# Optimization experiments

Measured on AMD Instinct MI355X. Metric: run time of the kernel, lower is better.

## Reference

```python
import jax, jax.numpy as jnp
import numpy as np

K_H, K_W = 3, 3
STRIDE, PAD = 1, 1
GN_GROUPS = 32
EPS = 1e-5


def setup_inputs() -> dict:
    key = jax.random.key(0)
    k1, k2, k3 = jax.random.split(key, 3)
    B, C, H, W = 4, 256, 64, 64
    Cout = 256
    x = jax.random.normal(k1, (B, C, H, W), jnp.float32)
    offset = jax.random.normal(k2, (B, 2 * K_H * K_W, H, W), jnp.float32)
    weight = jax.random.normal(k3, (Cout, C, K_H, K_W), jnp.float32) * 0.02
    gamma = jnp.ones((Cout,), jnp.float32)
    beta = jnp.zeros((Cout,), jnp.float32)
    return {"x": x, "offset": offset, "weight": weight, "gamma": gamma, "beta": beta}


def _deform_conv(x, offset, weight):
    B, C, H, W = x.shape
    Cout = weight.shape[0]
    K = K_H * K_W
    Ho = (H + 2 * PAD - K_H) // STRIDE + 1
    Wo = (W + 2 * PAD - K_W) // STRIDE + 1
    ky, kx = jnp.meshgrid(jnp.arange(K_H), jnp.arange(K_W), indexing='ij')
    ky = ky.reshape(K).astype(x.dtype)
    kx = kx.reshape(K).astype(x.dtype)
    # base sampling positions per kernel tap
    py_base = (jnp.arange(Ho) * STRIDE - PAD).astype(x.dtype)[None, :] + ky[:, None]  # [K,Ho]
    px_base = (jnp.arange(Wo) * STRIDE - PAD).astype(x.dtype)[None, :] + kx[:, None]  # [K,Wo]
    off = offset.reshape(B, K, 2, Ho, Wo)  # mmcv layout: (dy, dx) pairs per tap
    py = py_base[None, :, :, None] + off[:, :, 0]  # [B,K,Ho,Wo]
    px = px_base[None, :, None, :] + off[:, :, 1]  # [B,K,Ho,Wo]
    y0 = jnp.floor(py)
    x0 = jnp.floor(px)
    ly = py - y0
    lx = px - x0
    xf = x.reshape(B, C, H * W)

    def gather(yi, xi):
        valid = (yi >= 0) & (yi <= H - 1) & (xi >= 0) & (xi <= W - 1)
        yc = jnp.clip(yi, 0, H - 1).astype(jnp.int32)
        xc = jnp.clip(xi, 0, W - 1).astype(jnp.int32)
        idx = yc * W + xc  # [B,K,Ho,Wo]
        vals = jax.vmap(lambda xb, ib: xb[:, ib])(xf, idx)  # [B,C,K,Ho,Wo]
        return vals * valid[:, None].astype(x.dtype)

    g00 = gather(y0, x0)
    g01 = gather(y0, x0 + 1)
    g10 = gather(y0 + 1, x0)
    g11 = gather(y0 + 1, x0 + 1)
    wy = ly[:, None]  # [B,1,K,Ho,Wo]
    wx = lx[:, None]
    val = ((1 - wy) * (1 - wx) * g00 + (1 - wy) * wx * g01
           + wy * (1 - wx) * g10 + wy * wx * g11)  # [B,C,K,Ho,Wo]
    return jnp.einsum('bckhw,ock->bohw', val, weight.reshape(Cout, C, K))


def reference(x, offset, weight, gamma, beta):
    y = _deform_conv(x, offset, weight)  # [B,Cout,Ho,Wo]
    B, C, H, W = y.shape
    yg = y.reshape(B, GN_GROUPS, C // GN_GROUPS, H, W)
    mean = jnp.mean(yg, axis=(2, 3, 4), keepdims=True)
    var = jnp.var(yg, axis=(2, 3, 4), keepdims=True)
    yn = ((yg - mean) * jax.lax.rsqrt(var + EPS)).reshape(B, C, H, W)
    out = yn * gamma[None, :, None, None] + beta[None, :, None, None]
    return jax.nn.relu(out)
```

## Files before the change

kernel.cpp:

```cpp
#include <hip/hip_runtime.h>

typedef unsigned short ushort_t;
typedef __bf16 bf16x8 __attribute__((ext_vector_type(8)));
typedef float f32x4 __attribute__((ext_vector_type(4)));
typedef void __attribute__((address_space(1))) gvoid_t;
typedef void __attribute__((address_space(3))) lvoid_t;

__device__ __forceinline__ float bflo(unsigned u) { return __builtin_bit_cast(float, u << 16); }
__device__ __forceinline__ float bfhi(unsigned u) { return __builtin_bit_cast(float, u & 0xffff0000u); }
__device__ __forceinline__ unsigned f2bf_bits(float f) {
  unsigned u = __builtin_bit_cast(unsigned, f);
  return (u + 0x7fffu + ((u >> 16) & 1u)) >> 16;
}
__device__ __forceinline__ ushort_t f2bf(float f) { return (ushort_t)f2bf_bits(f); }

__global__ __launch_bounds__(256) void k_prep_w(const float* __restrict__ w,
                                                ushort_t* __restrict__ wb) {
  const int idx = blockIdx.x * 256 + threadIdx.x;
  const float* src = w + (size_t)idx * 9;
  #pragma unroll
  for (int k = 0; k < 9; ++k)
    wb[(k << 16) + idx] = f2bf(src[k]);
}

__global__ __launch_bounds__(256) void k_prep_x(const float* __restrict__ x,
                                                ushort_t* __restrict__ xt) {
  __shared__ ushort_t tile[64][68];
  const int bid = blockIdx.x;
  const int b = bid >> 8;
  const int ct = (bid >> 6) & 3;
  const int pt = bid & 63;
  const int t = threadIdx.x;
  const float* xb = x + ((size_t)(b * 256 + ct * 64)) * 4096 + pt * 64;
  #pragma unroll
  for (int i = 0; i < 16; ++i) {
    const int idx = t + 256 * i;
    const int c_l = idx >> 6, p_l = idx & 63;
    tile[c_l][p_l] = f2bf(xb[(size_t)c_l * 4096 + p_l]);
  }
  __syncthreads();
  ushort_t* xo = xt + ((size_t)(b * 4096 + pt * 64)) * 256 + ct * 64;
  #pragma unroll
  for (int i = 0; i < 16; ++i) {
    const int idx = t + 256 * i;
    const int p_l = idx >> 6, c_l = idx & 63;
    xo[(size_t)p_l * 256 + c_l] = tile[c_l][p_l];
  }
}

struct SMeta {
  float w00, w01, w10, w11;
  int i00, i01, i10, i11;
};
__device__ __forceinline__ SMeta meta_for(int h, int gw, int k, float oy, float ox) {
  SMeta m;
  const float py = (float)(h - 1 + k / 3) + oy;
  const float px = (float)(gw - 1 + k % 3) + ox;
  const float fy = floorf(py), fx = floorf(px);
  const float ly = py - fy, lx = px - fx;
  const int iy0 = (int)fy, ix0 = (int)fx;
  const float vy0 = (iy0 >= 0 && iy0 < 64) ? 1.f : 0.f;
  const float vy1 = (iy0 >= -1 && iy0 < 63) ? 1.f : 0.f;
  const float vx0 = (ix0 >= 0 && ix0 < 64) ? 1.f : 0.f;
  const float vx1 = (ix0 >= -1 && ix0 < 63) ? 1.f : 0.f;
  m.w00 = (1.f - ly) * (1.f - lx) * vy0 * vx0;
  m.w01 = (1.f - ly) * lx * vy0 * vx1;
  m.w10 = ly * (1.f - lx) * vy1 * vx0;
  m.w11 = ly * lx * vy1 * vx1;
  const int cy0 = min(max(iy0, 0), 63), cy1 = min(max(iy0 + 1, 0), 63);
  const int cx0 = min(max(ix0, 0), 63), cx1 = min(max(ix0 + 1, 0), 63);
  m.i00 = (cy0 * 64 + cx0) * 256;
  m.i01 = (cy0 * 64 + cx1) * 256;
  m.i10 = (cy1 * 64 + cx0) * 256;
  m.i11 = (cy1 * 64 + cx1) * 256;
  return m;
}

__device__ __forceinline__ unsigned lerp_pack(unsigned a, unsigned b, unsigned c, unsigned d,
                                              float w00, float w01, float w10, float w11) {
  float lo = w00 * bflo(a) + w01 * bflo(b) + w10 * bflo(c) + w11 * bflo(d);
  float hi = w00 * bfhi(a) + w01 * bfhi(b) + w10 * bfhi(c) + w11 * bfhi(d);
  return f2bf_bits(lo) | (f2bf_bits(hi) << 16);
}

__global__ __launch_bounds__(512) void k_gemm(const float* __restrict__ off,
                                              const ushort_t* __restrict__ xt,
                                              const ushort_t* __restrict__ wb,
                                              float* __restrict__ y,
                                              float* __restrict__ stats) {
  __shared__ __attribute__((aligned(16))) ushort_t Abuf[2][64 * 64];
  __shared__ __attribute__((aligned(16))) ushort_t Bbuf[2][256 * 64];

  const int bid = blockIdx.x;
  const int b = bid >> 6;
  const int h = bid & 63;
  const int t = threadIdx.x;
  const int wave = t >> 6;
  const int lane = t & 63;
  const int wq = lane >> 4;
  const int wr = lane & 15;
  const int wm = wave >> 2;
  const int wn = wave & 3;

  const int s_w = t >> 3;
  const int c8 = t & 7;

  const f32x4 zero = {0.f, 0.f, 0.f, 0.f};
  f32x4 acc[2][4];
  #pragma unroll
  for (int i = 0; i < 2; ++i)
    #pragma unroll
    for (int j = 0; j < 4; ++j) acc[i][j] = zero;

  const ushort_t* xtb = xt + (size_t)b * 4096 * 256;

  float offy[9], offx[9];
  {
    const float* offb = off + (size_t)b * 18 * 4096 + h * 64 + s_w;
    #pragma unroll
    for (int k = 0; k < 9; ++k) {
      offy[k] = offb[(2 * k) * 4096];
      offx[k] = offb[(2 * k + 1) * 4096];
    }
  }

  {
    const SMeta m = meta_for(h, s_w, 0, offy[0], offx[0]);
    const int cc = c8 * 8;
    const uint4 q00 = *(const uint4*)(xtb + m.i00 + cc);
    const uint4 q01 = *(const uint4*)(xtb + m.i01 + cc);
    const uint4 q10 = *(const uint4*)(xtb + m.i10 + cc);
    const uint4 q11 = *(const uint4*)(xtb + m.i11 + cc);
    #pragma unroll
    for (int i = 0; i < 4; ++i) {
      const int idx = i * 512 + t;
      const int row = idx >> 3, slot = idx & 7;
      const ushort_t* g = wb + row * 256 + ((slot ^ (row & 7)) << 3);
      __builtin_amdgcn_global_load_lds((gvoid_t*)g, (lvoid_t*)((char*)Bbuf[0] + idx * 16), 16, 0, 0);
    }
    uint4 r;
    r.x = lerp_pack(q00.x, q01.x, q10.x, q11.x, m.w00, m.w01, m.w10, m.w11);
    r.y = lerp_pack(q00.y, q01.y, q10.y, q11.y, m.w00, m.w01, m.w10, m.w11);
    r.z = lerp_pack(q00.z, q01.z, q10.z, q11.z, m.w00, m.w01, m.w10, m.w11);
    r.w = lerp_pack(q00.w, q01.w, q10.w, q11.w, m.w00, m.w01, m.w10, m.w11);
    *(uint4*)&Abuf[0][s_w * 64 + ((c8 ^ (s_w & 7)) << 3)] = r;
  }
  __syncthreads();

  #pragma unroll
  for (int n = 0; n < 36; ++n) {
    const int cur = n & 1;
    const int nb = cur ^ 1;
    uint4 q00, q01, q10, q11;
    SMeta m;
    if (n < 35) {
      const int kn = (n + 1) >> 2;
      const int c0n = ((n + 1) & 3) << 6;
      m = meta_for(h, s_w, kn, offy[kn], offx[kn]);
      const int cc = c0n + c8 * 8;
      q00 = *(const uint4*)(xtb + m.i00 + cc);
      q01 = *(const uint4*)(xtb + m.i01 + cc);
      q10 = *(const uint4*)(xtb + m.i10 + cc);
      q11 = *(const uint4*)(xtb + m.i11 + cc);
      #pragma unroll
      for (int i = 0; i < 4; ++i) {
        const int idx = i * 512 + t;
        const int row = idx >> 3, slot = idx & 7;
        const ushort_t* g = wb + (kn << 16) + row * 256 + c0n + ((slot ^ (row & 7)) << 3);
        __builtin_amdgcn_global_load_lds((gvoid_t*)g, (lvoid_t*)((char*)Bbuf[nb] + idx * 16), 16, 0, 0);
      }
    }
    #pragma unroll
    for (int ks = 0; ks < 2; ++ks) {
      bf16x8 af[2], bfr[4];
      #pragma unroll
      for (int tm = 0; tm < 2; ++tm) {
        const int row = wm * 32 + tm * 16 + wr;
        const int slot = (ks * 4 + wq) ^ (row & 7);
        af[tm] = *(const bf16x8*)&Abuf[cur][row * 64 + slot * 8];
      }
      #pragma unroll
      for (int tn = 0; tn < 4; ++tn) {
        const int row = wn * 64 + tn * 16 + wr;
        const int slot = (ks * 4 + wq) ^ (row & 7);
        bfr[tn] = *(const bf16x8*)&Bbuf[cur][row * 64 + slot * 8];
      }
      #pragma unroll
      for (int tm = 0; tm < 2; ++tm)
        #pragma unroll
        for (int tn = 0; tn < 4; ++tn)
          acc[tm][tn] =
              __builtin_amdgcn_mfma_f32_16x16x32_bf16(af[tm], bfr[tn], acc[tm][tn], 0, 0, 0);
    }
    if (n < 35) {
      uint4 r;
      r.x = lerp_pack(q00.x, q01.x, q10.x, q11.x, m.w00, m.w01, m.w10, m.w11);
      r.y = lerp_pack(q00.y, q01.y, q10.y, q11.y, m.w00, m.w01, m.w10, m.w11);
      r.z = lerp_pack(q00.z, q01.z, q10.z, q11.z, m.w00, m.w01, m.w10, m.w11);
      r.w = lerp_pack(q00.w, q01.w, q10.w, q11.w, m.w00, m.w01, m.w10, m.w11);
      *(uint4*)&Abuf[nb][s_w * 64 + ((c8 ^ (s_w & 7)) << 3)] = r;
    }
    __syncthreads();
  }

  float* yb = y + ((size_t)(b * 4096 + h * 64)) * 256;
  #pragma unroll
  for (int tm = 0; tm < 2; ++tm) {
    #pragma unroll
    for (int tn = 0; tn < 4; ++tn) {
      const int o = wn * 64 + tn * 16 + wr;
      #pragma unroll
      for (int r2 = 0; r2 < 4; ++r2) {
        const int ww = wm * 32 + tm * 16 + wq * 4 + r2;
        yb[ww * 256 + o] = acc[tm][tn][r2];
      }
    }
  }
  #pragma unroll
  for (int tn = 0; tn < 4; ++tn) {
    float sum = 0.f, ss = 0.f;
    #pragma unroll
    for (int tm = 0; tm < 2; ++tm)
      #pragma unroll
      for (int r2 = 0; r2 < 4; ++r2) {
        const float v = acc[tm][tn][r2];
        sum += v;
        ss += v * v;
      }
    sum += __shfl_xor(sum, 16, 64);
    ss += __shfl_xor(ss, 16, 64);
    sum += __shfl_xor(sum, 32, 64);
    ss += __shfl_xor(ss, 32, 64);
    #pragma unroll
    for (int d = 1; d < 8; d <<= 1) {
      sum += __shfl_xor(sum, d, 64);
      ss += __shfl_xor(ss, d, 64);
    }
    if (wq == 0 && (wr & 7) == 0) {
      const int g = wn * 8 + tn * 2 + (wr >> 3);
      atomicAdd(&stats[(b * 32 + g) * 2], sum);
      atomicAdd(&stats[(b * 32 + g) * 2 + 1], ss);
    }
  }
}

__global__ __launch_bounds__(256) void k_apply(const float* __restrict__ y,
                                               const float* __restrict__ stats,
                                               const float* __restrict__ gamma,
                                               const float* __restrict__ beta,
                                               float* __restrict__ out) {
  __shared__ float tile[64][65];
  __shared__ float sm[8], sr[8], sg[64], sb[64];
  const int bid = blockIdx.x;
  const int b = bid >> 8;
  const int st = (bid >> 2) & 63;
  const int ot = bid & 3;
  const int t = threadIdx.x;
  if (t < 8) {
    const int g = ot * 8 + t;
    const float s1 = stats[(b * 32 + g) * 2];
    const float s2 = stats[(b * 32 + g) * 2 + 1];
    const float mean = s1 * (1.f / 32768.f);
    const float var = s2 * (1.f / 32768.f) - mean * mean;
    sm[t] = mean;
    sr[t] = rsqrtf(var + 1e-5f);
  }
  if (t < 64) {
    sg[t] = gamma[ot * 64 + t];
    sb[t] = beta[ot * 64 + t];
  }
  const float* yb = y + ((size_t)(b * 4096 + st * 64)) * 256 + ot * 64;
  #pragma unroll
  for (int i = 0; i < 16; ++i) {
    const int idx = t + 256 * i;
    const int s_l = idx >> 6, o_l = idx & 63;
    tile[s_l][o_l] = yb[(size_t)s_l * 256 + o_l];
  }
  __syncthreads();
  float* ob = out + ((size_t)(b * 256 + ot * 64)) * 4096 + st * 64;
  #pragma unroll
  for (int i = 0; i < 16; ++i) {
    const int idx = t + 256 * i;
    const int o_l = idx >> 6, s_l = idx & 63;
    const int g = o_l >> 3;
    float v = (tile[s_l][o_l] - sm[g]) * sr[g] * sg[o_l] + sb[o_l];
    v = v > 0.f ? v : 0.f;
    ob[(size_t)o_l * 4096 + s_l] = v;
  }
}

extern "C" void kernel_launch(void* const* d_in, const int* in_sizes, int n_in,
                              void* d_out, int out_size, void* d_ws, size_t ws_size,
                              hipStream_t stream) {
  const float* x = (const float*)d_in[0];
  const float* off = (const float*)d_in[1];
  const float* w = (const float*)d_in[2];
  const float* gamma = (const float*)d_in[3];
  const float* beta = (const float*)d_in[4];
  float* out = (float*)d_out;

  char* ws = (char*)d_ws;
  float* y = (float*)(ws);
  ushort_t* xt = (ushort_t*)(ws + 16777216);
  ushort_t* wb = (ushort_t*)(ws + 25165824);
  float* stats = (float*)(ws + 26345472);

  hipMemsetAsync(stats, 0, 1024, stream);
  k_prep_w<<<256, 256, 0, stream>>>(w, wb);
  k_prep_x<<<1024, 256, 0, stream>>>(x, xt);
  k_gemm<<<256, 512, 0, stream>>>(off, xt, wb, y, stats);
  k_apply<<<1024, 256, 0, stream>>>(y, stats, gamma, beta, out);
}
```

Before: 97.41 us.

## Split GEMM K-loop across two 512-thread groups per block and remap block order

```diff
diff --git a/kernel.cpp b/kernel.cpp
--- a/kernel.cpp
+++ b/kernel.cpp
@@ -83,27 +83,31 @@
   return f2bf_bits(lo) | (f2bf_bits(hi) << 16);
 }
 
-__global__ __launch_bounds__(512) void k_gemm(const float* __restrict__ off,
-                                              const ushort_t* __restrict__ xt,
-                                              const ushort_t* __restrict__ wb,
-                                              float* __restrict__ y,
-                                              float* __restrict__ stats) {
-  __shared__ __attribute__((aligned(16))) ushort_t Abuf[2][64 * 64];
-  __shared__ __attribute__((aligned(16))) ushort_t Bbuf[2][256 * 64];
+__global__ __launch_bounds__(1024) void k_gemm(const float* __restrict__ off,
+                                               const ushort_t* __restrict__ xt,
+                                               const ushort_t* __restrict__ wb,
+                                               float* __restrict__ y,
+                                               float* __restrict__ stats) {
+  __shared__ __attribute__((aligned(16))) ushort_t Abuf[2][2][64 * 64];
+  __shared__ __attribute__((aligned(16))) ushort_t Bbuf[2][2][256 * 64];
 
   const int bid = blockIdx.x;
-  const int b = bid >> 6;
-  const int h = bid & 63;
+  const int lb = ((bid & 7) << 5) | (bid >> 3);
+  const int b = lb >> 6;
+  const int h = lb & 63;
   const int t = threadIdx.x;
+  const int g = t >> 9;
+  const int tl = t & 511;
   const int wave = t >> 6;
+  const int w8 = wave & 7;
   const int lane = t & 63;
   const int wq = lane >> 4;
   const int wr = lane & 15;
-  const int wm = wave >> 2;
-  const int wn = wave & 3;
-
-  const int s_w = t >> 3;
-  const int c8 = t & 7;
+  const int wm = w8 >> 2;
+  const int wn = w8 & 3;
+
+  const int s_w = tl >> 3;
+  const int c8 = tl & 7;
 
   const f32x4 zero = {0.f, 0.f, 0.f, 0.f};
   f32x4 acc[2][4];
@@ -113,61 +117,78 @@
     for (int j = 0; j < 4; ++j) acc[i][j] = zero;
 
   const ushort_t* xtb = xt + (size_t)b * 4096 * 256;
-
-  float offy[9], offx[9];
+  ushort_t* Ab = &Abuf[g][0][0];
+  ushort_t* Bb = &Bbuf[g][0][0];
+
+  float oy[5], ox[5];
   {
     const float* offb = off + (size_t)b * 18 * 4096 + h * 64 + s_w;
-    #pragma unroll
-    for (int k = 0; k < 9; ++k) {
-      offy[k] = offb[(2 * k) * 4096];
-      offx[k] = offb[(2 * k + 1) * 4096];
-    }
+    const int tapbase = g * 4;
+    #pragma unroll
+    for (int i = 0; i < 5; ++i) {
+      oy[i] = offb[(2 * (tapbase + i)) * 4096];
+      ox[i] = offb[(2 * (tapbase + i) + 1) * 4096];
+    }
+  }
+
+#define STAGE_ISSUE(TAP, LOC, C0, BDST)                                                      \
+  {                                                                                          \
+    m = meta_for(h, s_w, (TAP), oy[(LOC)], ox[(LOC)]);                                       \
+    const int cc = (C0) + c8 * 8;                                                            \
+    q00 = *(const uint4*)(xtb + m.i00 + cc);                                                 \
+    q01 = *(const uint4*)(xtb + m.i01 + cc);                                                 \
+    q10 = *(const uint4*)(xtb + m.i10 + cc);                                                 \
+    q11 = *(const uint4*)(xtb + m.i11 + cc);                                                 \
+    _Pragma("unroll") for (int i_ = 0; i_ < 4; ++i_) {                                       \
+      const int idx_ = i_ * 512 + tl;                                                        \
+      const int row_ = idx_ >> 3, slot_ = idx_ & 7;                                          \
+      const ushort_t* g_ = wb + ((TAP) << 16) + row_ * 256 + (C0) + ((slot_ ^ (row_ & 7)) << 3); \
+      __builtin_amdgcn_global_load_lds((gvoid_t*)g_, (lvoid_t*)((char*)(BDST) + idx_ * 16),  \
+                                       16, 0, 0);                                            \
+    }                                                                                        \
+  }
+
+#define STAGE_WRITE(ADST)                                               \
+  {                                                                     \
+    uint4 r;                                                            \
+    r.x = lerp_pack(q00.x, q01.x, q10.x, q11.x, m.w00, m.w01, m.w10, m.w11); \
+    r.y = lerp_pack(q00.y, q01.y, q10.y, q11.y, m.w00, m.w01, m.w10, m.w11); \
+    r.z = lerp_pack(q00.z, q01.z, q10.z, q11.z, m.w00, m.w01, m.w10, m.w11); \
+    r.w = lerp_pack(q00.w, q01.w, q10.w, q11.w, m.w00, m.w01, m.w10, m.w11); \
+    *(uint4*)&(ADST)[s_w * 64 + ((c8 ^ (s_w & 7)) << 3)] = r;           \
   }
 
   {
-    const SMeta m = meta_for(h, s_w, 0, offy[0], offx[0]);
-    const int cc = c8 * 8;
-    const uint4 q00 = *(const uint4*)(xtb + m.i00 + cc);
-    const uint4 q01 = *(const uint4*)(xtb + m.i01 + cc);
-    const uint4 q10 = *(const uint4*)(xtb + m.i10 + cc);
-    const uint4 q11 = *(const uint4*)(xtb + m.i11 + cc);
-    #pragma unroll
-    for (int i = 0; i < 4; ++i) {
-      const int idx = i * 512 + t;
-      const int row = idx >> 3, slot = idx & 7;
-      const ushort_t* g = wb + row * 256 + ((slot ^ (row & 7)) << 3);
-      __builtin_amdgcn_global_load_lds((gvoid_t*)g, (lvoid_t*)((char*)Bbuf[0] + idx * 16), 16, 0, 0);
-    }
-    uint4 r;
-    r.x = lerp_pack(q00.x, q01.x, q10.x, q11.x, m.w00, m.w01, m.w10, m.w11);
-    r.y = lerp_pack(q00.y, q01.y, q10.y, q11.y, m.w00, m.w01, m.w10, m.w11);
-    r.z = lerp_pack(q00.z, q01.z, q10.z, q11.z, m.w00, m.w01, m.w10, m.w11);
-    r.w = lerp_pack(q00.w, q01.w, q10.w, q11.w, m.w00, m.w01, m.w10, m.w11);
-    *(uint4*)&Abuf[0][s_w * 64 + ((c8 ^ (s_w & 7)) << 3)] = r;
+    uint4 q00, q01, q10, q11;
+    SMeta m;
+    if (g == 0) {
+      STAGE_ISSUE(0, 0, 0, &Bbuf[0][0][0]);
+      STAGE_WRITE(&Abuf[0][0][0]);
+    } else {
+      STAGE_ISSUE(4, 0, 128, &Bbuf[1][0][0]);
+      STAGE_WRITE(&Abuf[1][0][0]);
+    }
   }
   __syncthreads();
 
   #pragma unroll
-  for (int n = 0; n < 36; ++n) {
-    const int cur = n & 1;
+  for (int p = 0; p < 18; ++p) {
+    const int cur = p & 1;
     const int nb = cur ^ 1;
     uint4 q00, q01, q10, q11;
     SMeta m;
-    if (n < 35) {
-      const int kn = (n + 1) >> 2;
-      const int c0n = ((n + 1) & 3) << 6;
-      m = meta_for(h, s_w, kn, offy[kn], offx[kn]);
-      const int cc = c0n + c8 * 8;
-      q00 = *(const uint4*)(xtb + m.i00 + cc);
-      q01 = *(const uint4*)(xtb + m.i01 + cc);
-      q10 = *(const uint4*)(xtb + m.i10 + cc);
-      q11 = *(const uint4*)(xtb + m.i11 + cc);
-      #pragma unroll
-      for (int i = 0; i < 4; ++i) {
-        const int idx = i * 512 + t;
-        const int row = idx >> 3, slot = idx & 7;
-        const ushort_t* g = wb + (kn << 16) + row * 256 + c0n + ((slot ^ (row & 7)) << 3);
-        __builtin_amdgcn_global_load_lds((gvoid_t*)g, (lvoid_t*)((char*)Bbuf[nb] + idx * 16), 16, 0, 0);
+    if (p < 17) {
+      if (g == 0) {
+        const int n1 = p + 1;
+        const int tap = n1 >> 2;
+        const int c0n = (n1 & 3) << 6;
+        STAGE_ISSUE(tap, tap, c0n, (char*)Bb + nb * 32768);
+      } else {
+        const int n1 = 19 + p;
+        const int tap = n1 >> 2;
+        const int loc = tap - 4;
+        const int c0n = (n1 & 3) << 6;
+        STAGE_ISSUE(tap, loc, c0n, (char*)Bb + nb * 32768);
       }
     }
     #pragma unroll
@@ -177,13 +198,13 @@
       for (int tm = 0; tm < 2; ++tm) {
         const int row = wm * 32 + tm * 16 + wr;
         const int slot = (ks * 4 + wq) ^ (row & 7);
-        af[tm] = *(const bf16x8*)&Abuf[cur][row * 64 + slot * 8];
+        af[tm] = *(const bf16x8*)&Ab[cur * 4096 + row * 64 + slot * 8];
       }
       #pragma unroll
       for (int tn = 0; tn < 4; ++tn) {
         const int row = wn * 64 + tn * 16 + wr;
         const int slot = (ks * 4 + wq) ^ (row & 7);
-        bfr[tn] = *(const bf16x8*)&Bbuf[cur][row * 64 + slot * 8];
+        bfr[tn] = *(const bf16x8*)&Bb[cur * 16384 + row * 64 + slot * 8];
       }
       #pragma unroll
       for (int tm = 0; tm < 2; ++tm)
@@ -192,56 +213,74 @@
           acc[tm][tn] =
               __builtin_amdgcn_mfma_f32_16x16x32_bf16(af[tm], bfr[tn], acc[tm][tn], 0, 0, 0);
     }
-    if (n < 35) {
-      uint4 r;
-      r.x = lerp_pack(q00.x, q01.x, q10.x, q11.x, m.w00, m.w01, m.w10, m.w11);
-      r.y = lerp_pack(q00.y, q01.y, q10.y, q11.y, m.w00, m.w01, m.w10, m.w11);
-      r.z = lerp_pack(q00.z, q01.z, q10.z, q11.z, m.w00, m.w01, m.w10, m.w11);
-      r.w = lerp_pack(q00.w, q01.w, q10.w, q11.w, m.w00, m.w01, m.w10, m.w11);
-      *(uint4*)&Abuf[nb][s_w * 64 + ((c8 ^ (s_w & 7)) << 3)] = r;
+    if (p < 17) {
+      STAGE_WRITE(Ab + nb * 4096);
     }
     __syncthreads();
   }
 
-  float* yb = y + ((size_t)(b * 4096 + h * 64)) * 256;
-  #pragma unroll
-  for (int tm = 0; tm < 2; ++tm) {
+  float* comb = (float*)&Bbuf[0][0][0];
+  if (g == 1) {
+    #pragma unroll
+    for (int tm = 0; tm < 2; ++tm)
+      #pragma unroll
+      for (int tn = 0; tn < 4; ++tn)
+        #pragma unroll
+        for (int r2 = 0; r2 < 4; ++r2)
+          comb[(tm * 16 + tn * 4 + r2) * 512 + w8 * 64 + lane] = acc[tm][tn][r2];
+  }
+  __syncthreads();
+  if (g == 0) {
+    #pragma unroll
+    for (int tm = 0; tm < 2; ++tm)
+      #pragma unroll
+      for (int tn = 0; tn < 4; ++tn)
+        #pragma unroll
+        for (int r2 = 0; r2 < 4; ++r2)
+          acc[tm][tn][r2] += comb[(tm * 16 + tn * 4 + r2) * 512 + w8 * 64 + lane];
+
+    float* yb = y + ((size_t)(b * 4096 + h * 64)) * 256;
+    #pragma unroll
+    for (int tm = 0; tm < 2; ++tm) {
+      #pragma unroll
+      for (int tn = 0; tn < 4; ++tn) {
+        const int o = wn * 64 + tn * 16 + wr;
+        #pragma unroll
+        for (int r2 = 0; r2 < 4; ++r2) {
+          const int ww = wm * 32 + tm * 16 + wq * 4 + r2;
+          yb[ww * 256 + o] = acc[tm][tn][r2];
+        }
+      }
+    }
     #pragma unroll
     for (int tn = 0; tn < 4; ++tn) {
-      const int o = wn * 64 + tn * 16 + wr;
-      #pragma unroll
-      for (int r2 = 0; r2 < 4; ++r2) {
-        const int ww = wm * 32 + tm * 16 + wq * 4 + r2;
-        yb[ww * 256 + o] = acc[tm][tn][r2];
-      }
-    }
-  }
-  #pragma unroll
-  for (int tn = 0; tn < 4; ++tn) {
-    float sum = 0.f, ss = 0.f;
-    #pragma unroll
-    for (int tm = 0; tm < 2; ++tm)
-      #pragma unroll
-      for (int r2 = 0; r2 < 4; ++r2) {
-        const float v = acc[tm][tn][r2];
-        sum += v;
-        ss += v * v;
-      }
-    sum += __shfl_xor(sum, 16, 64);
-    ss += __shfl_xor(ss, 16, 64);
-    sum += __shfl_xor(sum, 32, 64);
-    ss += __shfl_xor(ss, 32, 64);
-    #pragma unroll
-    for (int d = 1; d < 8; d <<= 1) {
-      sum += __shfl_xor(sum, d, 64);
-      ss += __shfl_xor(ss, d, 64);
-    }
-    if (wq == 0 && (wr & 7) == 0) {
-      const int g = wn * 8 + tn * 2 + (wr >> 3);
-      atomicAdd(&stats[(b * 32 + g) * 2], sum);
-      atomicAdd(&stats[(b * 32 + g) * 2 + 1], ss);
-    }
-  }
+      float sum = 0.f, ss = 0.f;
+      #pragma unroll
+      for (int tm = 0; tm < 2; ++tm)
+        #pragma unroll
+        for (int r2 = 0; r2 < 4; ++r2) {
+          const float v = acc[tm][tn][r2];
+          sum += v;
+          ss += v * v;
+        }
+      sum += __shfl_xor(sum, 16, 64);
+      ss += __shfl_xor(ss, 16, 64);
+      sum += __shfl_xor(sum, 32, 64);
+      ss += __shfl_xor(ss, 32, 64);
+      #pragma unroll
+      for (int d = 1; d < 8; d <<= 1) {
+        sum += __shfl_xor(sum, d, 64);
+        ss += __shfl_xor(ss, d, 64);
+      }
+      if (wq == 0 && (wr & 7) == 0) {
+        const int gi = wn * 8 + tn * 2 + (wr >> 3);
+        atomicAdd(&stats[(b * 32 + gi) * 2], sum);
+        atomicAdd(&stats[(b * 32 + gi) * 2 + 1], ss);
+      }
+    }
+  }
+#undef STAGE_ISSUE
+#undef STAGE_WRITE
 }
 
 __global__ __launch_bounds__(256) void k_apply(const float* __restrict__ y,
@@ -252,9 +291,10 @@
   __shared__ float tile[64][65];
   __shared__ float sm[8], sr[8], sg[64], sb[64];
   const int bid = blockIdx.x;
-  const int b = bid >> 8;
-  const int st = (bid >> 2) & 63;
-  const int ot = bid & 3;
+  const int lb = ((bid & 7) << 7) | (bid >> 3);
+  const int b = lb >> 8;
+  const int st = (lb >> 2) & 63;
+  const int ot = lb & 3;
   const int t = threadIdx.x;
   if (t < 8) {
     const int g = ot * 8 + t;
@@ -308,6 +348,6 @@
   hipMemsetAsync(stats, 0, 1024, stream);
   k_prep_w<<<256, 256, 0, stream>>>(w, wb);
   k_prep_x<<<1024, 256, 0, stream>>>(x, xt);
-  k_gemm<<<256, 512, 0, stream>>>(off, xt, wb, y, stats);
+  k_gemm<<<256, 1024, 0, stream>>>(off, xt, wb, y, stats);
   k_apply<<<1024, 256, 0, stream>>>(y, stats, gamma, beta, out);
 }
```

Result: no change. 99.24 us (+1.9%).

## Triple-buffer weight tiles with manual waitcnt pipelining and XCD-aware block remap

Applied to the files above, without the earlier changes.

```diff
diff --git a/kernel.cpp b/kernel.cpp
--- a/kernel.cpp
+++ b/kernel.cpp
@@ -13,6 +13,9 @@
   return (u + 0x7fffu + ((u >> 16) & 1u)) >> 16;
 }
 __device__ __forceinline__ ushort_t f2bf(float f) { return (ushort_t)f2bf_bits(f); }
+
+#define VMWAIT(N) asm volatile("s_waitcnt vmcnt(" #N ")" ::: "memory")
+#define LGKM0 asm volatile("s_waitcnt lgkmcnt(0)" ::: "memory")
 
 __global__ __launch_bounds__(256) void k_prep_w(const float* __restrict__ w,
                                                 ushort_t* __restrict__ wb) {
@@ -89,11 +92,12 @@
                                               float* __restrict__ y,
                                               float* __restrict__ stats) {
   __shared__ __attribute__((aligned(16))) ushort_t Abuf[2][64 * 64];
-  __shared__ __attribute__((aligned(16))) ushort_t Bbuf[2][256 * 64];
+  __shared__ __attribute__((aligned(16))) ushort_t Bbuf[3][256 * 64];
 
   const int bid = blockIdx.x;
-  const int b = bid >> 6;
-  const int h = bid & 63;
+  const int lb = ((bid & 7) << 5) | (bid >> 3);
+  const int b = lb >> 6;
+  const int h = lb & 63;
   const int t = threadIdx.x;
   const int wave = t >> 6;
   const int lane = t & 63;
@@ -114,62 +118,73 @@
 
   const ushort_t* xtb = xt + (size_t)b * 4096 * 256;
 
-  float offy[9], offx[9];
+  float oy[9], ox[9];
   {
     const float* offb = off + (size_t)b * 18 * 4096 + h * 64 + s_w;
     #pragma unroll
     for (int k = 0; k < 9; ++k) {
-      offy[k] = offb[(2 * k) * 4096];
-      offx[k] = offb[(2 * k + 1) * 4096];
-    }
+      oy[k] = offb[(2 * k) * 4096];
+      ox[k] = offb[(2 * k + 1) * 4096];
+    }
+  }
+
+#define GATHER_ISSUE(TAP, C0)                             \
+  {                                                       \
+    m = meta_for(h, s_w, (TAP), oy[(TAP)], ox[(TAP)]);    \
+    const int cc = (C0) + c8 * 8;                         \
+    q00 = *(const uint4*)(xtb + m.i00 + cc);              \
+    q01 = *(const uint4*)(xtb + m.i01 + cc);              \
+    q10 = *(const uint4*)(xtb + m.i10 + cc);              \
+    q11 = *(const uint4*)(xtb + m.i11 + cc);              \
+  }
+
+#define B_ISSUE(TAP, C0, BUF)                                                                \
+  {                                                                                          \
+    _Pragma("unroll") for (int i_ = 0; i_ < 4; ++i_) {                                       \
+      const int idx_ = i_ * 512 + t;                                                         \
+      const int row_ = idx_ >> 3, slot_ = idx_ & 7;                                          \
+      const ushort_t* g_ = wb + ((TAP) << 16) + row_ * 256 + (C0) + ((slot_ ^ (row_ & 7)) << 3); \
+      __builtin_amdgcn_global_load_lds((gvoid_t*)g_,                                         \
+                                       (lvoid_t*)((char*)&Bbuf[(BUF)][0] + idx_ * 16), 16,   \
+                                       0, 0);                                                \
+    }                                                                                        \
+  }
+
+#define A_WRITE(BUF)                                                         \
+  {                                                                          \
+    uint4 r;                                                                 \
+    r.x = lerp_pack(q00.x, q01.x, q10.x, q11.x, m.w00, m.w01, m.w10, m.w11); \
+    r.y = lerp_pack(q00.y, q01.y, q10.y, q11.y, m.w00, m.w01, m.w10, m.w11); \
+    r.z = lerp_pack(q00.z, q01.z, q10.z, q11.z, m.w00, m.w01, m.w10, m.w11); \
+    r.w = lerp_pack(q00.w, q01.w, q10.w, q11.w, m.w00, m.w01, m.w10, m.w11); \
+    *(uint4*)&Abuf[(BUF)][s_w * 64 + ((c8 ^ (s_w & 7)) << 3)] = r;           \
   }
 
   {
-    const SMeta m = meta_for(h, s_w, 0, offy[0], offx[0]);
-    const int cc = c8 * 8;
-    const uint4 q00 = *(const uint4*)(xtb + m.i00 + cc);
-    const uint4 q01 = *(const uint4*)(xtb + m.i01 + cc);
-    const uint4 q10 = *(const uint4*)(xtb + m.i10 + cc);
-    const uint4 q11 = *(const uint4*)(xtb + m.i11 + cc);
-    #pragma unroll
-    for (int i = 0; i < 4; ++i) {
-      const int idx = i * 512 + t;
-      const int row = idx >> 3, slot = idx & 7;
-      const ushort_t* g = wb + row * 256 + ((slot ^ (row & 7)) << 3);
-      __builtin_amdgcn_global_load_lds((gvoid_t*)g, (lvoid_t*)((char*)Bbuf[0] + idx * 16), 16, 0, 0);
-    }
-    uint4 r;
-    r.x = lerp_pack(q00.x, q01.x, q10.x, q11.x, m.w00, m.w01, m.w10, m.w11);
-    r.y = lerp_pack(q00.y, q01.y, q10.y, q11.y, m.w00, m.w01, m.w10, m.w11);
-    r.z = lerp_pack(q00.z, q01.z, q10.z, q11.z, m.w00, m.w01, m.w10, m.w11);
-    r.w = lerp_pack(q00.w, q01.w, q10.w, q11.w, m.w00, m.w01, m.w10, m.w11);
-    *(uint4*)&Abuf[0][s_w * 64 + ((c8 ^ (s_w & 7)) << 3)] = r;
-  }
-  __syncthreads();
+    uint4 q00, q01, q10, q11;
+    SMeta m;
+    GATHER_ISSUE(0, 0);
+    B_ISSUE(0, 0, 0);
+    B_ISSUE(0, 64, 1);
+    VMWAIT(8);
+    A_WRITE(0);
+    LGKM0;
+    __builtin_amdgcn_s_barrier();
+  }
 
   #pragma unroll
   for (int n = 0; n < 36; ++n) {
-    const int cur = n & 1;
-    const int nb = cur ^ 1;
+    const int curB = n % 3;
+    const int curA = n & 1;
     uint4 q00, q01, q10, q11;
     SMeta m;
     if (n < 35) {
-      const int kn = (n + 1) >> 2;
-      const int c0n = ((n + 1) & 3) << 6;
-      m = meta_for(h, s_w, kn, offy[kn], offx[kn]);
-      const int cc = c0n + c8 * 8;
-      q00 = *(const uint4*)(xtb + m.i00 + cc);
-      q01 = *(const uint4*)(xtb + m.i01 + cc);
-      q10 = *(const uint4*)(xtb + m.i10 + cc);
-      q11 = *(const uint4*)(xtb + m.i11 + cc);
-      #pragma unroll
-      for (int i = 0; i < 4; ++i) {
-        const int idx = i * 512 + t;
-        const int row = idx >> 3, slot = idx & 7;
-        const ushort_t* g = wb + (kn << 16) + row * 256 + c0n + ((slot ^ (row & 7)) << 3);
-        __builtin_amdgcn_global_load_lds((gvoid_t*)g, (lvoid_t*)((char*)Bbuf[nb] + idx * 16), 16, 0, 0);
-      }
-    }
+      GATHER_ISSUE((n + 1) >> 2, ((n + 1) & 3) << 6);
+    }
+    if (n < 34) {
+      B_ISSUE((n + 2) >> 2, ((n + 2) & 3) << 6, (n + 2) % 3);
+    }
+    VMWAIT(12);
     #pragma unroll
     for (int ks = 0; ks < 2; ++ks) {
       bf16x8 af[2], bfr[4];
@@ -177,13 +192,13 @@
       for (int tm = 0; tm < 2; ++tm) {
         const int row = wm * 32 + tm * 16 + wr;
         const int slot = (ks * 4 + wq) ^ (row & 7);
-        af[tm] = *(const bf16x8*)&Abuf[cur][row * 64 + slot * 8];
+        af[tm] = *(const bf16x8*)&Abuf[curA][row * 64 + slot * 8];
       }
       #pragma unroll
       for (int tn = 0; tn < 4; ++tn) {
         const int row = wn * 64 + tn * 16 + wr;
         const int slot = (ks * 4 + wq) ^ (row & 7);
-        bfr[tn] = *(const bf16x8*)&Bbuf[cur][row * 64 + slot * 8];
+        bfr[tn] = *(const bf16x8*)&Bbuf[curB][row * 64 + slot * 8];
       }
       #pragma unroll
       for (int tm = 0; tm < 2; ++tm)
@@ -193,15 +208,19 @@
               __builtin_amdgcn_mfma_f32_16x16x32_bf16(af[tm], bfr[tn], acc[tm][tn], 0, 0, 0);
     }
     if (n < 35) {
-      uint4 r;
-      r.x = lerp_pack(q00.x, q01.x, q10.x, q11.x, m.w00, m.w01, m.w10, m.w11);
-      r.y = lerp_pack(q00.y, q01.y, q10.y, q11.y, m.w00, m.w01, m.w10, m.w11);
-      r.z = lerp_pack(q00.z, q01.z, q10.z, q11.z, m.w00, m.w01, m.w10, m.w11);
-      r.w = lerp_pack(q00.w, q01.w, q10.w, q11.w, m.w00, m.w01, m.w10, m.w11);
-      *(uint4*)&Abuf[nb][s_w * 64 + ((c8 ^ (s_w & 7)) << 3)] = r;
-    }
-    __syncthreads();
-  }
+      if (n == 34) {
+        VMWAIT(0);
+      } else {
+        VMWAIT(4);
+      }
+      A_WRITE((n + 1) & 1);
+      LGKM0;
+      __builtin_amdgcn_s_barrier();
+    }
+  }
+#undef GATHER_ISSUE
+#undef B_ISSUE
+#undef A_WRITE
 
   float* yb = y + ((size_t)(b * 4096 + h * 64)) * 256;
   #pragma unroll
@@ -237,9 +256,9 @@
       ss += __shfl_xor(ss, d, 64);
     }
     if (wq == 0 && (wr & 7) == 0) {
-      const int g = wn * 8 + tn * 2 + (wr >> 3);
-      atomicAdd(&stats[(b * 32 + g) * 2], sum);
-      atomicAdd(&stats[(b * 32 + g) * 2 + 1], ss);
+      const int gi = wn * 8 + tn * 2 + (wr >> 3);
+      atomicAdd(&stats[(b * 32 + gi) * 2], sum);
+      atomicAdd(&stats[(b * 32 + gi) * 2 + 1], ss);
     }
   }
 }
@@ -252,9 +271,10 @@
   __shared__ float tile[64][65];
   __shared__ float sm[8], sr[8], sg[64], sb[64];
   const int bid = blockIdx.x;
-  const int b = bid >> 8;
-  const int st = (bid >> 2) & 63;
-  const int ot = bid & 3;
+  const int lb = ((bid & 7) << 7) | (bid >> 3);
+  const int b = lb >> 8;
+  const int st = (lb >> 2) & 63;
+  const int ot = lb & 3;
   const int t = threadIdx.x;
   if (t < 8) {
     const int g = ot * 8 + t;
```

After: 93.75 us. -3.8%, faster.
